# Kernel optimization log

Measured on AMD Instinct MI355X. Metric: run time of the kernel, lower is better.

Reference implementation:

```python
import jax, jax.numpy as jnp
import numpy as np

N_NODES = 50000
N_EDGES = 800000
NODE_FEATURES = 128
HIDDEN = 64
N_CLASSES = 6


def gcn_conv(x, src, dst, W, b, n_nodes):
    """PyG GCNConv: out = D^{-1/2}(A+I)D^{-1/2} X W + b (self-loops included)."""
    deg = jax.ops.segment_sum(jnp.ones_like(dst, dtype=x.dtype), dst, num_segments=n_nodes)
    dinv = jnp.where(deg > 0, jax.lax.rsqrt(deg), 0.0)  # [N]
    h = x @ W  # [N, out] - transform before gather (fewer bytes moved)
    norm = dinv[src] * dinv[dst]  # [E+N]
    msg = h[src] * norm[:, None]  # [E+N, out]
    out = jax.ops.segment_sum(msg, dst, num_segments=n_nodes)  # [N, out]
    return out + b


def setup_inputs() -> dict:
    key = jax.random.key(0)
    ks = jax.random.split(key, 8)
    x = jax.random.normal(ks[0], (N_NODES, NODE_FEATURES), dtype=jnp.float32)
    edge_index = jax.random.randint(ks[1], (2, N_EDGES), 0, N_NODES, dtype=jnp.int64)
    W1 = jax.random.normal(ks[2], (NODE_FEATURES, HIDDEN), dtype=jnp.float32) * (1.0 / np.sqrt(NODE_FEATURES))
    b1 = jnp.zeros((HIDDEN,), dtype=jnp.float32)
    W2 = jax.random.normal(ks[3], (HIDDEN, HIDDEN), dtype=jnp.float32) * (1.0 / np.sqrt(HIDDEN))
    b2 = jnp.zeros((HIDDEN,), dtype=jnp.float32)
    Wc = jax.random.normal(ks[4], (HIDDEN * N_NODES, N_CLASSES), dtype=jnp.float32) * (1.0 / np.sqrt(HIDDEN * N_NODES))
    bc = jnp.zeros((N_CLASSES,), dtype=jnp.float32)
    return {"x": x, "edge_index": edge_index, "W1": W1, "b1": b1, "W2": W2, "b2": b2, "Wc": Wc, "bc": bc}


def reference(x, edge_index, W1, b1, W2, b2, Wc, bc):
    n_nodes = x.shape[0]
    loops = jnp.arange(n_nodes, dtype=edge_index.dtype)
    src = jnp.concatenate([edge_index[0], loops])
    dst = jnp.concatenate([edge_index[1], loops])
    h = jax.nn.relu(gcn_conv(x, src, dst, W1, b1, n_nodes))
    h = jax.nn.relu(gcn_conv(h, src, dst, W2, b2, n_nodes))
    logits = h.reshape(1, -1) @ Wc + bc  # [1, n_classes]
    return jax.nn.softmax(logits, axis=1)
```

## Files before the change

kernel.cpp:

```cpp
#include <hip/hip_runtime.h>
#include <math.h>


#define NCH 256
#define RBITS 10
#define NR_MAX 64

__device__ __forceinline__ ushort f32_to_bf16(float f) {
  unsigned u = __float_as_uint(f);
  return (ushort)((u + 0x7fffu + ((u >> 16) & 1u)) >> 16);
}
__device__ __forceinline__ float bf16_to_f32(ushort h) {
  return __uint_as_float(((unsigned)h) << 16);
}


__global__ __launch_bounds__(256) void hist_ranges(
    const int* __restrict__ dst, int* __restrict__ ghist, int NR, int E) {
  __shared__ int h[NR_MAX];
  int tid = threadIdx.x, c = blockIdx.x;
  if (tid < NR) h[tid] = 0;
  __syncthreads();
  int E4 = E >> 2;
  int CH4 = (E4 + NCH - 1) / NCH;
  int i0 = c * CH4, i1 = min(i0 + CH4, E4);
  const int4* d4 = (const int4*)dst;
  for (int i = i0 + tid; i < i1; i += 256) {
    int4 d = d4[i];
    atomicAdd(&h[d.x >> RBITS], 1);
    atomicAdd(&h[d.y >> RBITS], 1);
    atomicAdd(&h[d.z >> RBITS], 1);
    atomicAdd(&h[d.w >> RBITS], 1);
  }
  if (c == NCH - 1) {
    for (int e = (E4 << 2) + tid; e < E; e += 256) atomicAdd(&h[dst[e] >> RBITS], 1);
  }
  __syncthreads();
  if (tid < NR) ghist[tid * NCH + c] = h[tid];
}


__global__ __launch_bounds__(256) void scatter_ranges(
    const int* __restrict__ src, const int* __restrict__ dst,
    const int* __restrict__ ghist, int2* __restrict__ ebuf, int NR, int E) {
  __shared__ int cur[NR_MAX];
  __shared__ int rowpre[NR_MAX + 1];
  int tid = threadIdx.x, c = blockIdx.x;
  if (tid < NR) {
    const int4* row = (const int4*)(ghist + tid * NCH);
    int s = 0;
    for (int q = 0; q < NCH / 4; ++q) { int4 v = row[q]; s += v.x + v.y + v.z + v.w; }
    rowpre[tid + 1] = s;
  }
  __syncthreads();
  if (tid == 0) {
    rowpre[0] = 0;
    for (int i = 1; i <= NR; ++i) rowpre[i] += rowpre[i - 1];
  }
  __syncthreads();
  if (tid < NR) {
    int s = rowpre[tid];
    const int* row = ghist + tid * NCH;
    const int4* row4 = (const int4*)row;
    int c4 = c >> 2;
    for (int q = 0; q < c4; ++q) { int4 v = row4[q]; s += v.x + v.y + v.z + v.w; }
    for (int cc = c4 << 2; cc < c; ++cc) s += row[cc];
    cur[tid] = s;
  }
  __syncthreads();
  int E4 = E >> 2;
  int CH4 = (E4 + NCH - 1) / NCH;
  int i0 = c * CH4, i1 = min(i0 + CH4, E4);
  const int4* d4 = (const int4*)dst;
  const int4* s4 = (const int4*)src;
  for (int i = i0 + tid; i < i1; i += 256) {
    int4 d = d4[i];
    int4 s = s4[i];
    ebuf[atomicAdd(&cur[d.x >> RBITS], 1)] = make_int2(s.x, d.x);
    ebuf[atomicAdd(&cur[d.y >> RBITS], 1)] = make_int2(s.y, d.y);
    ebuf[atomicAdd(&cur[d.z >> RBITS], 1)] = make_int2(s.z, d.z);
    ebuf[atomicAdd(&cur[d.w >> RBITS], 1)] = make_int2(s.w, d.w);
  }
  if (c == NCH - 1) {
    for (int e = (E4 << 2) + tid; e < E; e += 256)
      ebuf[atomicAdd(&cur[dst[e] >> RBITS], 1)] = make_int2(src[e], dst[e]);
  }
}


__global__ __launch_bounds__(1024) void csr_range(
    const int2* __restrict__ ebuf, const int* __restrict__ ghist,
    int* __restrict__ offs, int* __restrict__ srt, float* __restrict__ dinv,
    int N, int E, int NR) {
  __shared__ int hist[1024];
  __shared__ int wtot[16];
  __shared__ int rowpre[NR_MAX + 1];
  int r = blockIdx.x;
  int lo = r << RBITS;
  int len = min(1024, N - lo);
  int tid = threadIdx.x, lane = tid & 63, wv = tid >> 6;
  if (tid < NR) {
    const int4* row = (const int4*)(ghist + tid * NCH);
    int s = 0;
    for (int q = 0; q < NCH / 4; ++q) { int4 v = row[q]; s += v.x + v.y + v.z + v.w; }
    rowpre[tid + 1] = s;
  }
  if (tid < len) hist[tid] = 0;
  __syncthreads();
  if (tid == 0) {
    rowpre[0] = 0;
    for (int i = 1; i <= NR; ++i) rowpre[i] += rowpre[i - 1];
  }
  __syncthreads();
  int S = rowpre[r], S1 = rowpre[r + 1];
  for (int i = S + tid; i < S1; i += 1024) atomicAdd(&hist[ebuf[i].y - lo], 1);
  __syncthreads();
  int v = (tid < len) ? hist[tid] : 0;
  if (tid < len) dinv[lo + tid] = rsqrtf((float)(v + 1));
  int x = v;
#pragma unroll
  for (int d = 1; d < 64; d <<= 1) { int y = __shfl_up(x, d, 64); if (lane >= d) x += y; }
  if (lane == 63) wtot[wv] = x;
  __syncthreads();
  if (wv == 0 && lane < 16) {
    int t = wtot[lane], xx = t;
#pragma unroll
    for (int d = 1; d < 16; d <<= 1) { int y = __shfl_up(xx, d, 64); if (lane >= d) xx += y; }
    wtot[lane] = xx - t;
  }
  __syncthreads();
  int excl = x - v + wtot[wv];
  if (tid < len) {
    offs[lo + tid] = S + excl;
    hist[tid] = S + excl;
  }
  if (r == 0 && tid == 0) offs[N] = E;
  __syncthreads();
  for (int i = S + tid; i < S1; i += 1024) {
    int2 e = ebuf[i];
    srt[atomicAdd(&hist[e.y - lo], 1)] = e.x;
  }
}


template <int K, int ROWS>
__global__ __launch_bounds__(256) void gemm_scale(
    const float* __restrict__ X, const float* __restrict__ W,
    const float* __restrict__ dinv, ushort* __restrict__ Gb, int N) {
  __shared__ float smw[K * 64];
  __shared__ float xs[ROWS * K];
  int tid = threadIdx.x, lane = tid & 63, wv = tid >> 6;
  for (int idx = tid; idx < K * 16; idx += 256)
    ((float4*)smw)[idx] = ((const float4*)W)[idx];
  int row0 = blockIdx.x * ROWS;
  int base = row0 * K;
  int cnt4 = (min(ROWS * K, N * K - base)) >> 2;
  const float4* X4 = (const float4*)(X + base);
  for (int idx = tid; idx < cnt4; idx += 256) ((float4*)xs)[idx] = X4[idx];
  __syncthreads();

  constexpr int RW = ROWS / 4;
  float acc[RW];
#pragma unroll
  for (int r = 0; r < RW; ++r) acc[r] = 0.f;
  const float* xr = &xs[(wv * RW) * K];
#pragma unroll 4
  for (int k = 0; k < K; ++k) {
    float wval = smw[k * 64 + lane];
#pragma unroll
    for (int r = 0; r < RW; ++r) acc[r] = fmaf(xr[r * K + k], wval, acc[r]);
  }
#pragma unroll
  for (int r = 0; r < RW; ++r) {
    int row = row0 + wv * RW + r;
    if (row < N) Gb[(size_t)row * 64 + lane] = f32_to_bf16(acc[r] * dinv[row]);
  }
}


template <int MODE>
__global__ __launch_bounds__(256) void aggregate(
    const ushort* __restrict__ Gb, const int* __restrict__ offs,
    const int* __restrict__ srt, const float* __restrict__ dinv,
    const float* __restrict__ bias, const float* __restrict__ Wx,
    ushort* __restrict__ Gout, float* __restrict__ part, int N) {
  int lane = threadIdx.x & 63, wv = threadIdx.x >> 6;
  int sub = lane >> 4, fl = lane & 15;
  int node = blockIdx.x * 4 + wv;
  const ushort4* G2 = (const ushort4*)Gb;

  if (MODE == 0 && node >= N) return;

  int e0 = 0, e1 = 0;
  if (node < N) { e0 = offs[node]; e1 = offs[node + 1]; }
  int deg = e1 - e0;

  float4 accA = make_float4(0.f, 0.f, 0.f, 0.f);
  float4 accB = make_float4(0.f, 0.f, 0.f, 0.f);
  if (sub == 0 && node < N) {
    ushort4 q = G2[(size_t)node * 16 + fl];
    accA.x = bf16_to_f32(q.x); accA.y = bf16_to_f32(q.y);
    accA.z = bf16_to_f32(q.z); accA.w = bf16_to_f32(q.w);
  }

  int pre = (deg > 0) ? srt[e0 + min(lane, deg - 1)] : 0;

  int dcap = min(deg, 64);
  int base = 0;
  for (; base + 7 < dcap; base += 8) {
    int sA = __shfl(pre, base + sub, 64);
    int sB = __shfl(pre, base + 4 + sub, 64);
    ushort4 qA = G2[(size_t)sA * 16 + fl];
    ushort4 qB = G2[(size_t)sB * 16 + fl];
    accA.x += bf16_to_f32(qA.x); accA.y += bf16_to_f32(qA.y);
    accA.z += bf16_to_f32(qA.z); accA.w += bf16_to_f32(qA.w);
    accB.x += bf16_to_f32(qB.x); accB.y += bf16_to_f32(qB.y);
    accB.z += bf16_to_f32(qB.z); accB.w += bf16_to_f32(qB.w);
  }
  for (; base + 3 < dcap; base += 4) {
    int s = __shfl(pre, base + sub, 64);
    ushort4 q = G2[(size_t)s * 16 + fl];
    accA.x += bf16_to_f32(q.x); accA.y += bf16_to_f32(q.y);
    accA.z += bf16_to_f32(q.z); accA.w += bf16_to_f32(q.w);
  }
  int e = e0 + base;
  for (; e + 3 < e1; e += 4) {
    int s = srt[e + sub];
    ushort4 q = G2[(size_t)s * 16 + fl];
    accA.x += bf16_to_f32(q.x); accA.y += bf16_to_f32(q.y);
    accA.z += bf16_to_f32(q.z); accA.w += bf16_to_f32(q.w);
  }
  int rem = e1 - e;
  if (sub < rem) {
    int s = srt[e + sub];
    ushort4 q = G2[(size_t)s * 16 + fl];
    accA.x += bf16_to_f32(q.x); accA.y += bf16_to_f32(q.y);
    accA.z += bf16_to_f32(q.z); accA.w += bf16_to_f32(q.w);
  }

  float4 acc;
  acc.x = accA.x + accB.x; acc.y = accA.y + accB.y;
  acc.z = accA.z + accB.z; acc.w = accA.w + accB.w;
#pragma unroll
  for (int m = 16; m < 64; m <<= 1) {
    acc.x += __shfl_xor(acc.x, m, 64);
    acc.y += __shfl_xor(acc.y, m, 64);
    acc.z += __shfl_xor(acc.z, m, 64);
    acc.w += __shfl_xor(acc.w, m, 64);
  }

  if (MODE == 0) {
    if (node < N) {
      float dn = dinv[node];
      float4 bb = ((const float4*)bias)[fl];
      float4 r;
      r.x = fmaxf(fmaf(acc.x, dn, bb.x), 0.f);
      r.y = fmaxf(fmaf(acc.y, dn, bb.y), 0.f);
      r.z = fmaxf(fmaf(acc.z, dn, bb.z), 0.f);
      r.w = fmaxf(fmaf(acc.w, dn, bb.w), 0.f);
      float4 o = make_float4(0.f, 0.f, 0.f, 0.f);
#pragma unroll
      for (int t = 0; t < 4; ++t) {
        int g = 4 * sub + t;
        int srcl = (lane & 48) | g;
        float h0 = __shfl(r.x, srcl, 64);
        float h1 = __shfl(r.y, srcl, 64);
        float h2 = __shfl(r.z, srcl, 64);
        float h3 = __shfl(r.w, srcl, 64);
        const float* wp = Wx + (size_t)(4 * g) * 64 + 4 * fl;
        float4 w0 = *(const float4*)(wp);
        float4 w1 = *(const float4*)(wp + 64);
        float4 w2 = *(const float4*)(wp + 128);
        float4 w3 = *(const float4*)(wp + 192);
        o.x = fmaf(h0, w0.x, fmaf(h1, w1.x, fmaf(h2, w2.x, fmaf(h3, w3.x, o.x))));
        o.y = fmaf(h0, w0.y, fmaf(h1, w1.y, fmaf(h2, w2.y, fmaf(h3, w3.y, o.y))));
        o.z = fmaf(h0, w0.z, fmaf(h1, w1.z, fmaf(h2, w2.z, fmaf(h3, w3.z, o.z))));
        o.w = fmaf(h0, w0.w, fmaf(h1, w1.w, fmaf(h2, w2.w, fmaf(h3, w3.w, o.w))));
      }
#pragma unroll
      for (int m = 16; m < 64; m <<= 1) {
        o.x += __shfl_xor(o.x, m, 64);
        o.y += __shfl_xor(o.y, m, 64);
        o.z += __shfl_xor(o.z, m, 64);
        o.w += __shfl_xor(o.w, m, 64);
      }
      if (sub == 0) {
        ushort4 q;
        q.x = f32_to_bf16(o.x * dn);
        q.y = f32_to_bf16(o.y * dn);
        q.z = f32_to_bf16(o.z * dn);
        q.w = f32_to_bf16(o.w * dn);
        ((ushort4*)Gout)[(size_t)node * 16 + fl] = q;
      }
    }
  } else {
    float a[6] = {0.f, 0.f, 0.f, 0.f, 0.f, 0.f};
    if (sub == 0 && node < N) {
      float dn = dinv[node];
      float4 bb = ((const float4*)bias)[fl];
      float4 r;
      r.x = fmaxf(fmaf(acc.x, dn, bb.x), 0.f);
      r.y = fmaxf(fmaf(acc.y, dn, bb.y), 0.f);
      r.z = fmaxf(fmaf(acc.z, dn, bb.z), 0.f);
      r.w = fmaxf(fmaf(acc.w, dn, bb.w), 0.f);
      const float4* w4 = (const float4*)(Wx + (size_t)node * 384 + fl * 24);
      float4 w0 = w4[0], w1 = w4[1], w2 = w4[2], w3 = w4[3], w4_ = w4[4], w5 = w4[5];
      a[0] = fmaf(r.x, w0.x, fmaf(r.y, w1.z, fmaf(r.z, w3.x, r.w * w4_.z)));
      a[1] = fmaf(r.x, w0.y, fmaf(r.y, w1.w, fmaf(r.z, w3.y, r.w * w4_.w)));
      a[2] = fmaf(r.x, w0.z, fmaf(r.y, w2.x, fmaf(r.z, w3.z, r.w * w5.x)));
      a[3] = fmaf(r.x, w0.w, fmaf(r.y, w2.y, fmaf(r.z, w3.w, r.w * w5.y)));
      a[4] = fmaf(r.x, w1.x, fmaf(r.y, w2.z, fmaf(r.z, w4_.x, r.w * w5.z)));
      a[5] = fmaf(r.x, w1.y, fmaf(r.y, w2.w, fmaf(r.z, w4_.y, r.w * w5.w)));
    }
#pragma unroll
    for (int c = 0; c < 6; ++c) {
      for (int d = 32; d > 0; d >>= 1) a[c] += __shfl_down(a[c], d, 64);
    }
    __shared__ float sh[4][6];
    if (lane == 0) {
#pragma unroll
      for (int c = 0; c < 6; ++c) sh[wv][c] = a[c];
    }
    __syncthreads();
    if (threadIdx.x == 0) {
#pragma unroll
      for (int c = 0; c < 6; ++c)
        part[(size_t)blockIdx.x * 6 + c] = sh[0][c] + sh[1][c] + sh[2][c] + sh[3][c];
    }
  }
}

__global__ __launch_bounds__(1024) void reduce_softmax(
    const float* __restrict__ part, int nb,
    const float* __restrict__ bc, float* __restrict__ out) {
  int tid = threadIdx.x, lane = tid & 63, wv = tid >> 6;
  float a[6] = {0.f, 0.f, 0.f, 0.f, 0.f, 0.f};
  for (int b = tid; b < nb; b += 1024) {
    const float* p = part + (size_t)b * 6;
#pragma unroll
    for (int c = 0; c < 6; ++c) a[c] += p[c];
  }
#pragma unroll
  for (int c = 0; c < 6; ++c) {
    for (int d = 32; d > 0; d >>= 1) a[c] += __shfl_down(a[c], d, 64);
  }
  __shared__ float sh[16][6];
  if (lane == 0) {
#pragma unroll
    for (int c = 0; c < 6; ++c) sh[wv][c] = a[c];
  }
  __syncthreads();
  if (tid == 0) {
    float l[6], m = -1e30f;
#pragma unroll
    for (int c = 0; c < 6; ++c) {
      float t = 0.f;
      for (int w = 0; w < 16; ++w) t += sh[w][c];
      l[c] = t + bc[c];
      m = fmaxf(m, l[c]);
    }
    float s = 0.f;
#pragma unroll
    for (int c = 0; c < 6; ++c) { l[c] = __expf(l[c] - m); s += l[c]; }
    float inv = 1.f / s;
#pragma unroll
    for (int c = 0; c < 6; ++c) out[c] = l[c] * inv;
  }
}


static inline size_t align4up(size_t x) { return (x + 3) & ~(size_t)3; }

extern "C" void kernel_launch(void* const* d_in, const int* in_sizes, int n_in,
                              void* d_out, int out_size, void* d_ws, size_t ws_size,
                              hipStream_t stream) {
  const float* x  = (const float*)d_in[0];
  const int*   ei = (const int*)d_in[1];
  const float* W1 = (const float*)d_in[2];
  const float* b1 = (const float*)d_in[3];
  const float* W2 = (const float*)d_in[4];
  const float* b2 = (const float*)d_in[5];
  const float* Wc = (const float*)d_in[6];
  const float* bc = (const float*)d_in[7];
  float* out = (float*)d_out;

  const int N = in_sizes[0] / 128;
  const int E = in_sizes[1] / 2;
  const int* esrc = ei;
  const int* edst = ei + E;
  const int NR = (N + 1023) >> RBITS;
  const int AGRID = (N + 3) / 4;

  size_t o = 0;
  int* offs   = (int*)d_ws + o;            o = align4up(o + N + 1);
  int* srt    = (int*)d_ws + o;            o = align4up(o + E);
  float* dinv = (float*)d_ws + o;          o = align4up(o + N);
  int* ghist  = (int*)d_ws + o;            o = align4up(o + (size_t)NR * NCH);
  ushort* Gb1 = (ushort*)((int*)d_ws + o); o = align4up(o + (size_t)N * 32);
  ushort* Gb2 = (ushort*)((int*)d_ws + o); o = align4up(o + max((size_t)N * 32, (size_t)E * 2));
  float* part = (float*)d_ws + o;          o = align4up(o + (size_t)AGRID * 6);
  int2* ebuf  = (int2*)Gb2;

  hist_ranges<<<NCH, 256, 0, stream>>>(edst, ghist, NR, E);
  scatter_ranges<<<NCH, 256, 0, stream>>>(esrc, edst, ghist, ebuf, NR, E);
  csr_range<<<NR, 1024, 0, stream>>>(ebuf, ghist, offs, srt, dinv, N, E, NR);

  gemm_scale<128, 32><<<(N + 31) / 32, 256, 0, stream>>>(x, W1, dinv, Gb1, N);
  aggregate<0><<<AGRID, 256, 0, stream>>>(Gb1, offs, srt, dinv, b1, W2, Gb2, nullptr, N);
  aggregate<1><<<AGRID, 256, 0, stream>>>(Gb2, offs, srt, dinv, b2, Wc, nullptr, part, N);

  reduce_softmax<<<1, 1024, 0, stream>>>(part, AGRID, bc, out);
}
```

Measured before the change: 159.7 us.

## Compress edge buffers to 16-bit indices and use finer destination ranges

The CSR build now uses 256-node destination ranges instead of 1024, so the per-range CSR kernel runs on about four times as many blocks. The intermediate edge buffer packs each source index and local destination into one 32-bit word instead of an int2. The sorted source list is stored as 16-bit values, which halves the index traffic in both aggregate passes. This relies on node ids fitting in 16 bits (N < 65536). It also adds a longer serial prefix loop over the larger number of ranges.

```diff
diff --git a/kernel.cpp b/kernel.cpp
--- a/kernel.cpp
+++ b/kernel.cpp
@@ -3,8 +3,8 @@
 
 
 #define NCH 256
-#define RBITS 10
-#define NR_MAX 64
+#define RBITS 8
+#define NR_MAX 256
 
 __device__ __forceinline__ ushort f32_to_bf16(float f) {
   unsigned u = __float_as_uint(f);
@@ -19,7 +19,7 @@
     const int* __restrict__ dst, int* __restrict__ ghist, int NR, int E) {
   __shared__ int h[NR_MAX];
   int tid = threadIdx.x, c = blockIdx.x;
-  if (tid < NR) h[tid] = 0;
+  for (int i = tid; i < NR; i += 256) h[i] = 0;
   __syncthreads();
   int E4 = E >> 2;
   int CH4 = (E4 + NCH - 1) / NCH;
@@ -36,13 +36,13 @@
     for (int e = (E4 << 2) + tid; e < E; e += 256) atomicAdd(&h[dst[e] >> RBITS], 1);
   }
   __syncthreads();
-  if (tid < NR) ghist[tid * NCH + c] = h[tid];
+  for (int i = tid; i < NR; i += 256) ghist[i * NCH + c] = h[i];
 }
 
 
 __global__ __launch_bounds__(256) void scatter_ranges(
     const int* __restrict__ src, const int* __restrict__ dst,
-    const int* __restrict__ ghist, int2* __restrict__ ebuf, int NR, int E) {
+    const int* __restrict__ ghist, int* __restrict__ ebuf, int NR, int E) {
   __shared__ int cur[NR_MAX];
   __shared__ int rowpre[NR_MAX + 1];
   int tid = threadIdx.x, c = blockIdx.x;
@@ -76,28 +76,28 @@
   for (int i = i0 + tid; i < i1; i += 256) {
     int4 d = d4[i];
     int4 s = s4[i];
-    ebuf[atomicAdd(&cur[d.x >> RBITS], 1)] = make_int2(s.x, d.x);
-    ebuf[atomicAdd(&cur[d.y >> RBITS], 1)] = make_int2(s.y, d.y);
-    ebuf[atomicAdd(&cur[d.z >> RBITS], 1)] = make_int2(s.z, d.z);
-    ebuf[atomicAdd(&cur[d.w >> RBITS], 1)] = make_int2(s.w, d.w);
+    ebuf[atomicAdd(&cur[d.x >> RBITS], 1)] = s.x | ((d.x & 255) << 16);
+    ebuf[atomicAdd(&cur[d.y >> RBITS], 1)] = s.y | ((d.y & 255) << 16);
+    ebuf[atomicAdd(&cur[d.z >> RBITS], 1)] = s.z | ((d.z & 255) << 16);
+    ebuf[atomicAdd(&cur[d.w >> RBITS], 1)] = s.w | ((d.w & 255) << 16);
   }
   if (c == NCH - 1) {
     for (int e = (E4 << 2) + tid; e < E; e += 256)
-      ebuf[atomicAdd(&cur[dst[e] >> RBITS], 1)] = make_int2(src[e], dst[e]);
+      ebuf[atomicAdd(&cur[dst[e] >> RBITS], 1)] = src[e] | ((dst[e] & 255) << 16);
   }
 }
 
 
 __global__ __launch_bounds__(1024) void csr_range(
-    const int2* __restrict__ ebuf, const int* __restrict__ ghist,
-    int* __restrict__ offs, int* __restrict__ srt, float* __restrict__ dinv,
+    const int* __restrict__ ebuf, const int* __restrict__ ghist,
+    int* __restrict__ offs, ushort* __restrict__ srt, float* __restrict__ dinv,
     int N, int E, int NR) {
-  __shared__ int hist[1024];
+  __shared__ int hist[NR_MAX];
   __shared__ int wtot[16];
   __shared__ int rowpre[NR_MAX + 1];
   int r = blockIdx.x;
   int lo = r << RBITS;
-  int len = min(1024, N - lo);
+  int len = min(1 << RBITS, N - lo);
   int tid = threadIdx.x, lane = tid & 63, wv = tid >> 6;
   if (tid < NR) {
     const int4* row = (const int4*)(ghist + tid * NCH);
@@ -113,7 +113,7 @@
   }
   __syncthreads();
   int S = rowpre[r], S1 = rowpre[r + 1];
-  for (int i = S + tid; i < S1; i += 1024) atomicAdd(&hist[ebuf[i].y - lo], 1);
+  for (int i = S + tid; i < S1; i += 1024) atomicAdd(&hist[ebuf[i] >> 16], 1);
   __syncthreads();
   int v = (tid < len) ? hist[tid] : 0;
   if (tid < len) dinv[lo + tid] = rsqrtf((float)(v + 1));
@@ -137,8 +137,8 @@
   if (r == 0 && tid == 0) offs[N] = E;
   __syncthreads();
   for (int i = S + tid; i < S1; i += 1024) {
-    int2 e = ebuf[i];
-    srt[atomicAdd(&hist[e.y - lo], 1)] = e.x;
+    int e = ebuf[i];
+    srt[atomicAdd(&hist[e >> 16], 1)] = (ushort)(e & 0xFFFF);
   }
 }
 
@@ -181,7 +181,7 @@
 template <int MODE>
 __global__ __launch_bounds__(256) void aggregate(
     const ushort* __restrict__ Gb, const int* __restrict__ offs,
-    const int* __restrict__ srt, const float* __restrict__ dinv,
+    const ushort* __restrict__ srt, const float* __restrict__ dinv,
     const float* __restrict__ bias, const float* __restrict__ Wx,
     ushort* __restrict__ Gout, float* __restrict__ part, int N) {
   int lane = threadIdx.x & 63, wv = threadIdx.x >> 6;
@@ -203,7 +203,7 @@
     accA.z = bf16_to_f32(q.z); accA.w = bf16_to_f32(q.w);
   }
 
-  int pre = (deg > 0) ? srt[e0 + min(lane, deg - 1)] : 0;
+  int pre = (deg > 0) ? (int)srt[e0 + min(lane, deg - 1)] : 0;
 
   int dcap = min(deg, 64);
   int base = 0;
@@ -388,18 +388,18 @@
   const int E = in_sizes[1] / 2;
   const int* esrc = ei;
   const int* edst = ei + E;
-  const int NR = (N + 1023) >> RBITS;
+  const int NR = (N + (1 << RBITS) - 1) >> RBITS;
   const int AGRID = (N + 3) / 4;
 
   size_t o = 0;
-  int* offs   = (int*)d_ws + o;            o = align4up(o + N + 1);
-  int* srt    = (int*)d_ws + o;            o = align4up(o + E);
-  float* dinv = (float*)d_ws + o;          o = align4up(o + N);
-  int* ghist  = (int*)d_ws + o;            o = align4up(o + (size_t)NR * NCH);
-  ushort* Gb1 = (ushort*)((int*)d_ws + o); o = align4up(o + (size_t)N * 32);
-  ushort* Gb2 = (ushort*)((int*)d_ws + o); o = align4up(o + max((size_t)N * 32, (size_t)E * 2));
-  float* part = (float*)d_ws + o;          o = align4up(o + (size_t)AGRID * 6);
-  int2* ebuf  = (int2*)Gb2;
+  int* offs    = (int*)d_ws + o;            o = align4up(o + N + 1);
+  ushort* srt  = (ushort*)((int*)d_ws + o); o = align4up(o + (E + 1) / 2);
+  float* dinv  = (float*)d_ws + o;          o = align4up(o + N);
+  int* ghist   = (int*)d_ws + o;            o = align4up(o + (size_t)NR * NCH);
+  ushort* Gb1  = (ushort*)((int*)d_ws + o); o = align4up(o + (size_t)N * 32);
+  ushort* Gb2  = (ushort*)((int*)d_ws + o); o = align4up(o + max((size_t)N * 32, (size_t)E));
+  float* part  = (float*)d_ws + o;          o = align4up(o + (size_t)AGRID * 6);
+  int* ebuf    = (int*)Gb2;
 
   hist_ranges<<<NCH, 256, 0, stream>>>(edst, ghist, NR, E);
   scatter_ranges<<<NCH, 256, 0, stream>>>(esrc, edst, ghist, ebuf, NR, E);
```

Result: no change. 157.7 us (-1.3%).
